# Performance work log

Hardware: AMD Instinct MI355X
Metric: run time of the kernel (lower is better)

The kernel has to match this reference:

```python
import jax, jax.numpy as jnp
import numpy as np

B, H, W, C = 16, 56, 56, 512
NH, WS, SS = 16, 7, 3
N = WS * WS
NW = (H // WS) * (W // WS)
HD = C // NH
SCALE = HD ** -0.5
MLP_H = 4 * C


def _rel_index():
    coords = np.stack(np.meshgrid(np.arange(WS), np.arange(WS), indexing='ij'))  # (2, Ws, Ws)
    cf = coords.reshape(2, -1)
    rel = (cf[:, :, None] - cf[:, None, :]).transpose(1, 2, 0)  # (N, N, 2)
    rel[:, :, 0] += WS - 1
    rel[:, :, 1] += WS - 1
    rel[:, :, 0] *= 2 * WS - 1
    return rel.sum(-1)  # (N, N)

REL_IDX = jnp.asarray(_rel_index())


def _attn_mask():
    img = np.zeros((H, W), np.int32)
    cnt = 0
    for hs in (slice(0, H - WS), slice(H - WS, H - SS), slice(H - SS, H)):
        for ws_ in (slice(0, W - WS), slice(W - WS, W - SS), slice(W - SS, W)):
            img[hs, ws_] = cnt
            cnt += 1
    mw = img.reshape(H // WS, WS, W // WS, WS).transpose(0, 2, 1, 3).reshape(NW, N)
    am = mw[:, None, :] - mw[:, :, None]
    return jnp.asarray(np.where(am != 0, -100.0, 0.0).astype(np.float32))  # (nW, N, N)

ATTN_MASK = _attn_mask()


def _ln(x, g, b):
    mu = x.mean(-1, keepdims=True)
    var = ((x - mu) ** 2).mean(-1, keepdims=True)
    return (x - mu) / jnp.sqrt(var + 1e-5) * g + b


def _partition(x):  # (B,H,W,C) -> (B*nW, N, C)
    return x.reshape(B, H // WS, WS, W // WS, WS, C).transpose(0, 1, 3, 2, 4, 5).reshape(-1, N, C)


def _reverse(xw):  # (B*nW, N, C) -> (B,H,W,C)
    return xw.reshape(B, H // WS, W // WS, WS, WS, C).transpose(0, 1, 3, 2, 4, 5).reshape(B, H, W, C)


def _qkv(x, qw, qb):
    qkv = (x @ qw.T + qb).reshape(-1, N, 3, NH, HD).transpose(2, 0, 3, 1, 4)
    return qkv[0], qkv[1], qkv[2]  # each (B*nW, NH, N, HD)


def setup_inputs() -> dict:
    key = jax.random.key(0)
    ks = jax.random.split(key, 8)
    s = 0.02
    return {
        'x1': jax.random.normal(ks[0], (B, H * W, C), jnp.float32),
        'x2': jax.random.normal(ks[1], (B, H * W, C), jnp.float32),
        'norm1_g': jnp.ones((C,), jnp.float32),
        'norm1_b': jnp.zeros((C,), jnp.float32),
        'qkv_w': jax.random.normal(ks[2], (3 * C, C), jnp.float32) * s,
        'qkv_b': jnp.zeros((3 * C,), jnp.float32),
        'rel_tab': jax.random.normal(ks[3], ((2 * WS - 1) ** 2, NH), jnp.float32) * s,
        'proj_w': jax.random.normal(ks[4], (C, C), jnp.float32) * s,
        'proj_b': jnp.zeros((C,), jnp.float32),
        'norm2_g': jnp.ones((C,), jnp.float32),
        'norm2_b': jnp.zeros((C,), jnp.float32),
        'fc1_w': jax.random.normal(ks[5], (MLP_H, C), jnp.float32) * s,
        'fc1_b': jnp.zeros((MLP_H,), jnp.float32),
        'fc2_w': jax.random.normal(ks[6], (C, MLP_H), jnp.float32) * s,
        'fc2_b': jnp.zeros((C,), jnp.float32),
    }


def reference(x1, x2, norm1_g, norm1_b, qkv_w, qkv_b, rel_tab, proj_w, proj_b,
              norm2_g, norm2_b, fc1_w, fc1_b, fc2_w, fc2_b):
    shortcut = x1
    a1 = _ln(x1, norm1_g, norm1_b).reshape(B, H, W, C)
    a2 = _ln(x2, norm1_g, norm1_b).reshape(B, H, W, C)
    # cyclic shift (SW-MSA)
    a1 = jnp.roll(a1, (-SS, -SS), axis=(1, 2))
    a2 = jnp.roll(a2, (-SS, -SS), axis=(1, 2))
    w1 = _partition(a1)
    w2 = _partition(a2)
    q1, k1, v1 = _qkv(w1, qkv_w, qkv_b)
    _, k2, v2 = _qkv(w2, qkv_w, qkv_b)
    q1 = q1 * SCALE
    # gather relative position bias: (NH, N, N)
    bias = rel_tab[REL_IDX.reshape(-1)].reshape(N, N, NH).transpose(2, 0, 1)
    attn1 = jnp.einsum('bhnd,bhmd->bhnm', q1, k1) + bias[None]
    attn2 = jnp.einsum('bhnd,bhmd->bhnm', q1, k2) + bias[None]
    m = ATTN_MASK[None, :, None]  # (1, nW, 1, N, N)
    attn1 = (attn1.reshape(B, NW, NH, N, N) + m).reshape(-1, NH, N, N)
    attn2 = (attn2.reshape(B, NW, NH, N, N) + m).reshape(-1, NH, N, N)
    attn = jax.nn.softmax(jnp.concatenate([attn1, attn2], axis=1), axis=-1)  # (B*nW, 2NH, N, N)
    v = jnp.concatenate([v1, v2], axis=1)  # (B*nW, 2NH, N, HD)
    xw = jnp.einsum('bhnm,bhmd->bhnd', attn, v).transpose(0, 2, 1, 3).reshape(-1, N, 2 * C)
    weights = xw
    xw = xw[:, :, :C] @ proj_w.T + proj_b
    x = _reverse(xw)
    x = jnp.roll(x, (SS, SS), axis=(1, 2)).reshape(B, H * W, C)
    x = shortcut + x
    y = _ln(x, norm2_g, norm2_b)
    y = jax.nn.gelu(y @ fc1_w.T + fc1_b, approximate=False) @ fc2_w.T + fc2_b
    return x + y
```

## Files before the change

kernel.cpp:

```cpp
#include <hip/hip_runtime.h>
#include <math.h>

typedef __attribute__((ext_vector_type(8))) short short8;
typedef __attribute__((ext_vector_type(4))) float floatx4;

#define TOKENS 50176
#define HTOK   25088

__device__ __forceinline__ unsigned short f2bf(float f) {
  union { float f; unsigned int i; } x; x.f = f;
  unsigned int r = x.i + 0x7fffu + ((x.i >> 16) & 1u);
  return (unsigned short)(r >> 16);
}
__device__ __forceinline__ float bf2f(unsigned short u) {
  union { unsigned int i; float f; } x; x.i = ((unsigned int)u) << 16; return x.f;
}

__device__ __forceinline__ void gload16(const void* g, void* l) {
  __builtin_amdgcn_global_load_lds(
      (__attribute__((address_space(1))) void*)g,
      (__attribute__((address_space(3))) void*)l, 16, 0, 0);
}

__global__ __launch_bounds__(256) void wcvt(
    const float* __restrict__ src, unsigned short* __restrict__ dst, int n8) {
  int i = blockIdx.x * 256 + threadIdx.x;
  if (i >= n8) return;
  const float* p = src + (size_t)i * 8;
  floatx4 a = *(const floatx4*)p;
  floatx4 b = *(const floatx4*)(p + 4);
  short8 o;
#pragma unroll
  for (int k = 0; k < 4; ++k) { o[k] = (short)f2bf(a[k]); o[k + 4] = (short)f2bf(b[k]); }
  *(short8*)(dst + (size_t)i * 8) = o;
}

__global__ __launch_bounds__(256) void prep_ln1(
    const float* __restrict__ x1, const float* __restrict__ g,
    const float* __restrict__ b, unsigned short* __restrict__ a1w) {
  int gw = (blockIdx.x * 256 + threadIdx.x) >> 6;
  int lane = threadIdx.x & 63;
  if (gw >= TOKENS) return;
  int n = gw % 49, w = gw / 49;
  int i = n / 7, j = n % 7;
  int ww = w & 7, wh = (w >> 3) & 7, bb = w >> 6;
  int hs = (wh * 7 + i + 3) % 56;
  int wsS = (ww * 7 + j + 3) % 56;
  const float* rp = x1 + ((size_t)bb * 3136 + (size_t)hs * 56 + wsS) * 512 + lane * 8;
  floatx4 a0 = *(const floatx4*)rp;
  floatx4 a1 = *(const floatx4*)(rp + 4);
  float s = 0.f, ss = 0.f;
#pragma unroll
  for (int k = 0; k < 4; ++k) { s += a0[k]; ss += a0[k] * a0[k]; }
#pragma unroll
  for (int k = 0; k < 4; ++k) { s += a1[k]; ss += a1[k] * a1[k]; }
  for (int m = 32; m >= 1; m >>= 1) {
    s  += __shfl_xor(s, m, 64);
    ss += __shfl_xor(ss, m, 64);
  }
  float mu = s * (1.f / 512.f);
  float var = ss * (1.f / 512.f) - mu * mu;
  float rstd = rsqrtf(var + 1e-5f);
  floatx4 g0 = *(const floatx4*)(g + lane * 8);
  floatx4 g1 = *(const floatx4*)(g + lane * 8 + 4);
  floatx4 b0 = *(const floatx4*)(b + lane * 8);
  floatx4 b1 = *(const floatx4*)(b + lane * 8 + 4);
  short8 o8;
#pragma unroll
  for (int k = 0; k < 4; ++k) {
    o8[k]     = (short)f2bf((a0[k] - mu) * rstd * g0[k] + b0[k]);
    o8[k + 4] = (short)f2bf((a1[k] - mu) * rstd * g1[k] + b1[k]);
  }
  *(short8*)(a1w + (size_t)gw * 512 + lane * 8) = o8;
}

__global__ __launch_bounds__(256) void ln2_apply(
    const float* __restrict__ xin, const float* __restrict__ g,
    const float* __restrict__ b, unsigned short* __restrict__ outb) {
  int gw = (blockIdx.x * 256 + threadIdx.x) >> 6;
  int lane = threadIdx.x & 63;
  if (gw >= TOKENS) return;
  const float* rp = xin + (size_t)gw * 512 + lane * 8;
  floatx4 a0 = *(const floatx4*)rp;
  floatx4 a1 = *(const floatx4*)(rp + 4);
  float s = 0.f, ss = 0.f;
#pragma unroll
  for (int k = 0; k < 4; ++k) { s += a0[k]; ss += a0[k] * a0[k]; }
#pragma unroll
  for (int k = 0; k < 4; ++k) { s += a1[k]; ss += a1[k] * a1[k]; }
  for (int m = 32; m >= 1; m >>= 1) {
    s  += __shfl_xor(s, m, 64);
    ss += __shfl_xor(ss, m, 64);
  }
  float mu = s * (1.f / 512.f);
  float var = ss * (1.f / 512.f) - mu * mu;
  float rstd = rsqrtf(var + 1e-5f);
  floatx4 g0 = *(const floatx4*)(g + lane * 8);
  floatx4 g1 = *(const floatx4*)(g + lane * 8 + 4);
  floatx4 b0 = *(const floatx4*)(b + lane * 8);
  floatx4 b1 = *(const floatx4*)(b + lane * 8 + 4);
  short8 o8;
#pragma unroll
  for (int k = 0; k < 4; ++k) {
    o8[k]     = (short)f2bf((a0[k] - mu) * rstd * g0[k] + b0[k]);
    o8[k + 4] = (short)f2bf((a1[k] - mu) * rstd * g1[k] + b1[k]);
  }
  *(short8*)(outb + (size_t)gw * 512 + lane * 8) = o8;
}

template <int EPI>
__global__ __launch_bounds__(256, 2) void gemm_glds(
    const unsigned short* __restrict__ A,
    const unsigned short* __restrict__ Bw,
    const float* __restrict__ bias,
    void* __restrict__ outp,
    const float* __restrict__ res,
    int N, int K, int lda) {
  __shared__ unsigned short lA[128 * 64];
  __shared__ unsigned short lB[128 * 64];
  int tid = threadIdx.x;
  int wave = tid >> 6, lane = tid & 63;

  int srow = wave * 32 + (lane >> 3);
  int scol = (lane & 7) * 8;
  const unsigned short* gA[4];
  const unsigned short* gB[4];
#pragma unroll
  for (int i = 0; i < 4; ++i) {
    gA[i] = A + (size_t)(blockIdx.x * 128 + srow + i * 8) * lda + scol;
    gB[i] = Bw + (size_t)(blockIdx.y * 128 + srow + i * 8) * K + scol;
  }
  unsigned short* lAp = &lA[wave * 2048];
  unsigned short* lBp = &lB[wave * 2048];

  int wm = (wave >> 1) * 64, wn = (wave & 1) * 64;
  int l15 = lane & 15, kq = (lane >> 4) * 8;
  int KT = K >> 6;
  floatx4 acc[4][4] = {};

  for (int kt = 0; kt < KT; ++kt) {
    int ko = kt * 64;
#pragma unroll
    for (int i = 0; i < 4; ++i) {
      gload16(gA[i] + ko, lAp + i * 512);
      gload16(gB[i] + ko, lBp + i * 512);
    }
    __syncthreads();
#pragma unroll
    for (int ks = 0; ks < 2; ++ks) {
      short8 af[4], bf8[4];
#pragma unroll
      for (int tm = 0; tm < 4; ++tm)
        af[tm] = *(const short8*)&lA[(wm + tm * 16 + l15) * 64 + ks * 32 + kq];
#pragma unroll
      for (int tn = 0; tn < 4; ++tn)
        bf8[tn] = *(const short8*)&lB[(wn + tn * 16 + l15) * 64 + ks * 32 + kq];
#pragma unroll
      for (int tm = 0; tm < 4; ++tm)
#pragma unroll
        for (int tn = 0; tn < 4; ++tn)
          acc[tm][tn] = __builtin_amdgcn_mfma_f32_16x16x32_bf16(
              af[tm], bf8[tn], acc[tm][tn], 0, 0, 0);
    }
    __syncthreads();
  }

  int colb = blockIdx.y * 128 + wn + l15;
  int rowb = blockIdx.x * 128 + wm + ((lane >> 4) << 2);
#pragma unroll
  for (int tm = 0; tm < 4; ++tm) {
#pragma unroll
    for (int rg = 0; rg < 4; ++rg) {
      int m = rowb + tm * 16 + rg;
      size_t outrow;
      const float* resrow = nullptr;
      if (EPI == 1) {
        int nn = m % 49, wI = m / 49;
        int i = nn / 7, j = nn % 7;
        int wwI = wI & 7, whI = (wI >> 3) & 7, bb = wI >> 6;
        int hs = (whI * 7 + i + 3) % 56;
        int wsS = (wwI * 7 + j + 3) % 56;
        size_t orig = (size_t)bb * 3136 + (size_t)hs * 56 + wsS;
        outrow = orig * 512;
        resrow = res + orig * 512;
      } else {
        outrow = (size_t)m * N;
        if (EPI == 3) resrow = res + (size_t)m * 512;
      }
#pragma unroll
      for (int tn = 0; tn < 4; ++tn) {
        int n = colb + tn * 16;
        float v = acc[tm][tn][rg] + bias[n];
        if (EPI == 2) v = 0.5f * v * (1.f + erff(v * 0.70710678118654752f));
        if (EPI == 0 || EPI == 2) {
          ((unsigned short*)outp)[outrow + n] = f2bf(v);
        } else {
          ((float*)outp)[outrow + n] = v + resrow[n];
        }
      }
    }
  }
}

__global__ __launch_bounds__(256) void attn_kernel(
    unsigned short* qkv,
    const float* __restrict__ rel_tab) {
  __shared__ float ldsK[4][49 * 32];
  __shared__ float ldsV[4][49 * 32];
  int wg = blockIdx.x;
  int wave = threadIdx.x >> 6, lane = threadIdx.x & 63;
  int wh = (wg >> 3) & 7, ww = wg & 7;
  int r = lane;
  int ir = r / 7, jr = r % 7;
  int rh = (wh < 7) ? 0 : ((ir < 4) ? 1 : 2);
  int rw = (ww < 7) ? 0 : ((jr < 4) ? 1 : 2);
  int labr = rh * 3 + rw;
  const size_t base = (size_t)wg * 49 * 1536;

  for (int hh = 0; hh < 4; ++hh) {
    int head = wave * 4 + hh;
    __syncthreads();
    for (int idx = lane; idx < 49 * 32; idx += 64) {
      int rr = idx >> 5, d = idx & 31;
      size_t ro = base + (size_t)rr * 1536 + head * 32 + d;
      ldsK[wave][idx] = bf2f(qkv[ro + 512]);
      ldsV[wave][idx] = bf2f(qkv[ro + 1024]);
    }
    __syncthreads();
    if (r < 49) {
      float qf[32];
#pragma unroll
      for (int d8 = 0; d8 < 4; ++d8) {
        short8 raw = *(const short8*)(qkv + base + (size_t)r * 1536 + head * 32 + d8 * 8);
#pragma unroll
        for (int k = 0; k < 8; ++k) qf[d8 * 8 + k] = bf2f((unsigned short)raw[k]);
      }
      float sarr[49];
      float mx = -1e30f;
#pragma unroll
      for (int c = 0; c < 49; ++c) {
        float dot = 0.f;
#pragma unroll
        for (int d = 0; d < 32; ++d) dot += qf[d] * ldsK[wave][c * 32 + d];
        int ic = c / 7, jc = c % 7;
        int ch = (wh < 7) ? 0 : ((ic < 4) ? 1 : 2);
        int cw = (ww < 7) ? 0 : ((jc < 4) ? 1 : 2);
        float mask = ((ch * 3 + cw) != labr) ? -100.f : 0.f;
        int ridx = (ir - ic + 6) * 13 + (jr - jc + 6);
        float sv = dot * 0.17677669529663687f + rel_tab[ridx * 16 + head] + mask;
        sarr[c] = sv;
        mx = fmaxf(mx, sv);
      }
      float sum = 0.f;
#pragma unroll
      for (int c = 0; c < 49; ++c) { float e = __expf(sarr[c] - mx); sarr[c] = e; sum += e; }
      float inv = 1.f / sum;
      float o[32];
#pragma unroll
      for (int d = 0; d < 32; ++d) o[d] = 0.f;
#pragma unroll
      for (int c = 0; c < 49; ++c) {
        float p = sarr[c];
#pragma unroll
        for (int d = 0; d < 32; ++d) o[d] += p * ldsV[wave][c * 32 + d];
      }
      unsigned short* dst = qkv + base + (size_t)r * 1536 + head * 32;
#pragma unroll
      for (int d8 = 0; d8 < 4; ++d8) {
        short8 pk;
#pragma unroll
        for (int k = 0; k < 8; ++k) pk[k] = (short)f2bf(o[d8 * 8 + k] * inv);
        *(short8*)(dst + d8 * 8) = pk;
      }
    }
  }
}

extern "C" void kernel_launch(void* const* d_in, const int* in_sizes, int n_in,
                              void* d_out, int out_size, void* d_ws, size_t ws_size,
                              hipStream_t stream) {
  const float* x1     = (const float*)d_in[0];
  const float* n1g    = (const float*)d_in[2];
  const float* n1b    = (const float*)d_in[3];
  const float* qkv_w  = (const float*)d_in[4];
  const float* qkv_b  = (const float*)d_in[5];
  const float* rel_t  = (const float*)d_in[6];
  const float* proj_w = (const float*)d_in[7];
  const float* proj_b = (const float*)d_in[8];
  const float* n2g    = (const float*)d_in[9];
  const float* n2b    = (const float*)d_in[10];
  const float* fc1_w  = (const float*)d_in[11];
  const float* fc1_b  = (const float*)d_in[12];
  const float* fc2_w  = (const float*)d_in[13];
  const float* fc2_b  = (const float*)d_in[14];
  float* outp = (float*)d_out;

  char* ws = (char*)d_ws;
  unsigned short* a1w    = (unsigned short*)ws;
  unsigned short* bufQ   = (unsigned short*)(ws + 51380224);
  unsigned short* pwbf   = (unsigned short*)ws;
  unsigned short* f1wbf  = (unsigned short*)(ws + 524288);
  unsigned short* f2wbf  = (unsigned short*)(ws + 2621440);
  unsigned short* xln2   = (unsigned short*)(ws + 4718592);
  unsigned short* hbuf   = (unsigned short*)(ws + 56098816);
  unsigned short* qkvwbf = (unsigned short*)d_out;

  wcvt<<<384, 256, 0, stream>>>(qkv_w, qkvwbf, 98304);
  prep_ln1<<<TOKENS / 4, 256, 0, stream>>>(x1, n1g, n1b, a1w);
  gemm_glds<0><<<dim3(392, 12), 256, 0, stream>>>(
      a1w, qkvwbf, qkv_b, bufQ, nullptr, 1536, 512, 512);
  wcvt<<<128, 256, 0, stream>>>(proj_w, pwbf, 32768);
  wcvt<<<512, 256, 0, stream>>>(fc1_w, f1wbf, 131072);
  wcvt<<<512, 256, 0, stream>>>(fc2_w, f2wbf, 131072);
  attn_kernel<<<1024, 256, 0, stream>>>(bufQ, rel_t);
  gemm_glds<1><<<dim3(392, 4), 256, 0, stream>>>(
      bufQ, pwbf, proj_b, outp, x1, 512, 512, 1536);
  ln2_apply<<<TOKENS / 4, 256, 0, stream>>>(outp, n2g, n2b, xln2);
  for (int ch = 0; ch < 2; ++ch) {
    size_t ro = (size_t)ch * HTOK * 512;
    gemm_glds<2><<<dim3(196, 16), 256, 0, stream>>>(
        xln2 + ro, f1wbf, fc1_b, hbuf, nullptr, 2048, 512, 512);
    gemm_glds<3><<<dim3(196, 4), 256, 0, stream>>>(
        hbuf, f2wbf, fc2_b, outp + ro, outp + ro, 512, 2048, 2048);
  }
}
```

Before: 1.047 ms.

## Rewrite window attention with MFMA bf16 matmuls and one head per wave

After: 990.2 us. 5.4% less time.

```diff
diff --git a/kernel.cpp b/kernel.cpp
--- a/kernel.cpp
+++ b/kernel.cpp
@@ -20,6 +20,12 @@
   __builtin_amdgcn_global_load_lds(
       (__attribute__((address_space(1))) void*)g,
       (__attribute__((address_space(3))) void*)l, 16, 0, 0);
+}
+
+__device__ __forceinline__ unsigned cvtpk(float lo, float hi) {
+  unsigned r;
+  asm("v_cvt_pk_bf16_f32 %0, %1, %2" : "=v"(r) : "v"(lo), "v"(hi));
+  return r;
 }
 
 __global__ __launch_bounds__(256) void wcvt(
@@ -202,75 +208,178 @@
   }
 }
 
-__global__ __launch_bounds__(256) void attn_kernel(
+__global__ __launch_bounds__(256, 3) void attn_mfma(
     unsigned short* qkv,
-    const float* __restrict__ rel_tab) {
-  __shared__ float ldsK[4][49 * 32];
-  __shared__ float ldsV[4][49 * 32];
-  int wg = blockIdx.x;
+    const float* __restrict__ relt) {
+  __shared__ unsigned short ldsVt[4][32 * 72];
+  __shared__ unsigned short ldsP[4][4096];
   int wave = threadIdx.x >> 6, lane = threadIdx.x & 63;
-  int wh = (wg >> 3) & 7, ww = wg & 7;
-  int r = lane;
-  int ir = r / 7, jr = r % 7;
-  int rh = (wh < 7) ? 0 : ((ir < 4) ? 1 : 2);
-  int rw = (ww < 7) ? 0 : ((jr < 4) ? 1 : 2);
-  int labr = rh * 3 + rw;
-  const size_t base = (size_t)wg * 49 * 1536;
-
-  for (int hh = 0; hh < 4; ++hh) {
-    int head = wave * 4 + hh;
-    __syncthreads();
-    for (int idx = lane; idx < 49 * 32; idx += 64) {
-      int rr = idx >> 5, d = idx & 31;
-      size_t ro = base + (size_t)rr * 1536 + head * 32 + d;
-      ldsK[wave][idx] = bf2f(qkv[ro + 512]);
-      ldsV[wave][idx] = bf2f(qkv[ro + 1024]);
-    }
-    __syncthreads();
-    if (r < 49) {
-      float qf[32];
-#pragma unroll
-      for (int d8 = 0; d8 < 4; ++d8) {
-        short8 raw = *(const short8*)(qkv + base + (size_t)r * 1536 + head * 32 + d8 * 8);
-#pragma unroll
-        for (int k = 0; k < 8; ++k) qf[d8 * 8 + k] = bf2f((unsigned short)raw[k]);
-      }
-      float sarr[49];
-      float mx = -1e30f;
-#pragma unroll
-      for (int c = 0; c < 49; ++c) {
-        float dot = 0.f;
-#pragma unroll
-        for (int d = 0; d < 32; ++d) dot += qf[d] * ldsK[wave][c * 32 + d];
-        int ic = c / 7, jc = c % 7;
-        int ch = (wh < 7) ? 0 : ((ic < 4) ? 1 : 2);
-        int cw = (ww < 7) ? 0 : ((jc < 4) ? 1 : 2);
-        float mask = ((ch * 3 + cw) != labr) ? -100.f : 0.f;
-        int ridx = (ir - ic + 6) * 13 + (jr - jc + 6);
-        float sv = dot * 0.17677669529663687f + rel_tab[ridx * 16 + head] + mask;
-        sarr[c] = sv;
-        mx = fmaxf(mx, sv);
-      }
-      float sum = 0.f;
-#pragma unroll
-      for (int c = 0; c < 49; ++c) { float e = __expf(sarr[c] - mx); sarr[c] = e; sum += e; }
-      float inv = 1.f / sum;
-      float o[32];
-#pragma unroll
-      for (int d = 0; d < 32; ++d) o[d] = 0.f;
-#pragma unroll
-      for (int c = 0; c < 49; ++c) {
-        float p = sarr[c];
-#pragma unroll
-        for (int d = 0; d < 32; ++d) o[d] += p * ldsV[wave][c * 32 + d];
-      }
-      unsigned short* dst = qkv + base + (size_t)r * 1536 + head * 32;
-#pragma unroll
-      for (int d8 = 0; d8 < 4; ++d8) {
-        short8 pk;
-#pragma unroll
-        for (int k = 0; k < 8; ++k) pk[k] = (short)f2bf(o[d8 * 8 + k] * inv);
-        *(short8*)(dst + d8 * 8) = pk;
+  int win = blockIdx.x >> 2, hg = blockIdx.x & 3;
+  int head = hg * 4 + wave;
+  int l15 = lane & 15, rg = lane >> 4;
+  int wh = (win >> 3) & 7, ww = win & 7;
+  const size_t base = (size_t)win * 49 * 1536;
+
+  short8 vreg[4];
+#pragma unroll
+  for (int c = 0; c < 4; ++c) {
+    int p = c >> 1, kh = c & 1;
+    int k = kh * 32 + (lane >> 1);
+    int kr = k < 49 ? k : 48;
+    vreg[c] = *(const short8*)(qkv + base + (size_t)kr * 1536 + head * 32 +
+                               1024 + p * 16 + (lane & 1) * 8);
+  }
+
+  int iq[4], jq[4], rq[4];
+#pragma unroll
+  for (int tn = 0; tn < 4; ++tn) {
+    int q = tn * 16 + l15;
+    int i7 = (q * 9363) >> 16;
+    iq[tn] = i7; jq[tn] = q - i7 * 7;
+    int rh = (wh < 7) ? 0 : ((i7 < 4) ? 1 : 2);
+    int rw = (ww < 7) ? 0 : ((jq[tn] < 4) ? 1 : 2);
+    rq[tn] = rh * 3 + rw;
+  }
+  unsigned ridx4[16];
+  unsigned long long mbits = 0ull;
+  unsigned validb = 0;
+#pragma unroll
+  for (int tm = 0; tm < 4; ++tm) {
+#pragma unroll
+    for (int rr = 0; rr < 4; ++rr) {
+      int e = tm * 4 + rr;
+      int k = tm * 16 + rg * 4 + rr;
+      int ik = (k * 9363) >> 16;
+      int jk = k - ik * 7;
+      int rhk = (wh < 7) ? 0 : ((ik < 4) ? 1 : 2);
+      int rwk = (ww < 7) ? 0 : ((jk < 4) ? 1 : 2);
+      int rk = rhk * 3 + rwk;
+      if (k < 49) validb |= (1u << e);
+      unsigned pack = 0;
+#pragma unroll
+      for (int tn = 0; tn < 4; ++tn) {
+        int ridx = (iq[tn] - ik + 6) * 13 + (jq[tn] - jk + 6);
+        ridx = ridx < 0 ? 0 : (ridx > 168 ? 168 : ridx);
+        pack |= (unsigned)ridx << (8 * tn);
+        if (rq[tn] != rk) mbits |= 1ull << (e * 4 + tn);
+      }
+      ridx4[e] = pack;
+    }
+  }
+
+  short8 kf[4], qf[4];
+#pragma unroll
+  for (int t = 0; t < 4; ++t) {
+    int r = t * 16 + l15; r = r < 49 ? r : 48;
+    kf[t] = *(const short8*)(qkv + base + (size_t)r * 1536 + head * 32 + 512 + rg * 8);
+    qf[t] = *(const short8*)(qkv + base + (size_t)r * 1536 + head * 32 + rg * 8);
+  }
+  floatx4 acc[4][4] = {};
+#pragma unroll
+  for (int tm = 0; tm < 4; ++tm)
+#pragma unroll
+    for (int tn = 0; tn < 4; ++tn)
+      acc[tm][tn] = __builtin_amdgcn_mfma_f32_16x16x32_bf16(
+          kf[tm], qf[tn], acc[tm][tn], 0, 0, 0);
+
+  unsigned short* vt = &ldsVt[wave][0];
+#pragma unroll
+  for (int c = 0; c < 4; ++c) {
+    int p = c >> 1, kh = c & 1;
+    int k = kh * 32 + (lane >> 1);
+    int d0 = p * 16 + (lane & 1) * 8;
+#pragma unroll
+    for (int j = 0; j < 8; ++j)
+      vt[(d0 + j) * 72 + k] = (unsigned short)vreg[c][j];
+  }
+
+  float mrow[4] = {-3e38f, -3e38f, -3e38f, -3e38f};
+#pragma unroll
+  for (int tm = 0; tm < 4; ++tm) {
+#pragma unroll
+    for (int rr = 0; rr < 4; ++rr) {
+      int e = tm * 4 + rr;
+      bool val = (validb >> e) & 1;
+#pragma unroll
+      for (int tn = 0; tn < 4; ++tn) {
+        float bias = relt[((ridx4[e] >> (8 * tn)) & 255u) * 16 + head];
+        float mk = ((mbits >> (e * 4 + tn)) & 1ull) ? -100.f : 0.f;
+        float v = val ? fmaf(acc[tm][tn][rr], 0.17677669529663687f, bias + mk)
+                      : -1e30f;
+        acc[tm][tn][rr] = v;
+        mrow[tn] = fmaxf(mrow[tn], v);
+      }
+    }
+  }
+#pragma unroll
+  for (int tn = 0; tn < 4; ++tn) {
+    mrow[tn] = fmaxf(mrow[tn], __shfl_xor(mrow[tn], 16, 64));
+    mrow[tn] = fmaxf(mrow[tn], __shfl_xor(mrow[tn], 32, 64));
+  }
+  float ssum[4] = {0.f, 0.f, 0.f, 0.f};
+#pragma unroll
+  for (int tm = 0; tm < 4; ++tm)
+#pragma unroll
+    for (int tn = 0; tn < 4; ++tn)
+#pragma unroll
+      for (int rr = 0; rr < 4; ++rr) {
+        float e = __expf(acc[tm][tn][rr] - mrow[tn]);
+        acc[tm][tn][rr] = e;
+        ssum[tn] += e;
+      }
+#pragma unroll
+  for (int tn = 0; tn < 4; ++tn) {
+    ssum[tn] += __shfl_xor(ssum[tn], 16, 64);
+    ssum[tn] += __shfl_xor(ssum[tn], 32, 64);
+  }
+  float inv[4];
+#pragma unroll
+  for (int tn = 0; tn < 4; ++tn) inv[tn] = 1.f / ssum[tn];
+
+  char* pb = (char*)&ldsP[wave][0];
+#pragma unroll
+  for (int tm = 0; tm < 4; ++tm) {
+#pragma unroll
+    for (int tn = 0; tn < 4; ++tn) {
+      unsigned lo = cvtpk(acc[tm][tn][0] * inv[tn], acc[tm][tn][1] * inv[tn]);
+      unsigned hi = cvtpk(acc[tm][tn][2] * inv[tn], acc[tm][tn][3] * inv[tn]);
+      int q = tn * 16 + l15;
+      int off = (q * 128 + tm * 32 + rg * 8) ^ ((q & 7) << 4);
+      *(unsigned long long*)(pb + off) = ((unsigned long long)hi << 32) | lo;
+    }
+  }
+
+  floatx4 o[4][2] = {};
+#pragma unroll
+  for (int ks = 0; ks < 2; ++ks) {
+    short8 af[4], vf[2];
+#pragma unroll
+    for (int qt = 0; qt < 4; ++qt) {
+      int q = qt * 16 + l15;
+      int off = (q * 128 + ks * 64 + rg * 16) ^ ((q & 7) << 4);
+      af[qt] = *(const short8*)(pb + off);
+    }
+#pragma unroll
+    for (int dt = 0; dt < 2; ++dt)
+      vf[dt] = *(const short8*)&ldsVt[wave][(dt * 16 + l15) * 72 + ks * 32 + rg * 8];
+#pragma unroll
+    for (int qt = 0; qt < 4; ++qt)
+#pragma unroll
+      for (int dt = 0; dt < 2; ++dt)
+        o[qt][dt] = __builtin_amdgcn_mfma_f32_16x16x32_bf16(
+            af[qt], vf[dt], o[qt][dt], 0, 0, 0);
+  }
+
+#pragma unroll
+  for (int qt = 0; qt < 4; ++qt) {
+#pragma unroll
+    for (int rr = 0; rr < 4; ++rr) {
+      int q = qt * 16 + rg * 4 + rr;
+      if (q < 49) {
+#pragma unroll
+        for (int dt = 0; dt < 2; ++dt)
+          qkv[base + (size_t)q * 1536 + head * 32 + dt * 16 + l15] =
+              f2bf(o[qt][dt][rr]);
       }
     }
   }
@@ -312,7 +421,7 @@
   wcvt<<<128, 256, 0, stream>>>(proj_w, pwbf, 32768);
   wcvt<<<512, 256, 0, stream>>>(fc1_w, f1wbf, 131072);
   wcvt<<<512, 256, 0, stream>>>(fc2_w, f2wbf, 131072);
-  attn_kernel<<<1024, 256, 0, stream>>>(bufQ, rel_t);
+  attn_mfma<<<4096, 256, 0, stream>>>(bufQ, rel_t);
   gemm_glds<1><<<dim3(392, 4), 256, 0, stream>>>(
       bufQ, pwbf, proj_b, outp, x1, 512, 512, 1536);
   ln2_apply<<<TOKENS / 4, 256, 0, stream>>>(outp, n2g, n2b, xln2);
```
